# Kernel tuning notes

Measured on AMD Instinct MI355X. Metric: run time of the kernel, lower is better.

Reference implementation:

```python
import jax, jax.numpy as jnp
import numpy as np
import math

B, N, E, H, D = 8, 1024, 1024, 16, 64  # batch, node_cnt, embedding_dim, head_num, qkv_dim
SQRT_E, SQRT_D, CLIP = 32.0, 8.0, 10.0
MAX_PERIOD = 10000.0


def setup_inputs() -> dict:
    key = jax.random.key(0)
    ks = jax.random.split(key, 16)
    s = 0.03  # weight scale keeps tanh/softmax in a sane range
    return {
        "t": jax.random.uniform(ks[0], (B,), jnp.float32),
        "encoded_jobs": jax.random.normal(ks[1], (B, N, E), jnp.float32) * 0.5,
        "xt": jax.random.uniform(ks[2], (B, N, N), jnp.float32),
        "Wq": jax.random.normal(ks[3], (H * D, E), jnp.float32) * s,
        "Wk": jax.random.normal(ks[4], (H * D, E), jnp.float32) * s,
        "Wv": jax.random.normal(ks[5], (H * D, E), jnp.float32) * s,
        "Wc": jax.random.normal(ks[6], (E, H * D), jnp.float32) * s,
        "bc": jnp.zeros((E,), jnp.float32),
        "conv_w": jax.random.normal(ks[7], (2, 2), jnp.float32) * 0.5,  # 1x1 Conv2d(2,2)
        "conv_b": jnp.zeros((2,), jnp.float32),
        "tW1": jax.random.normal(ks[8], (E // 2, E), jnp.float32) * s,
        "tb1": jnp.zeros((E // 2,), jnp.float32),
        "tW2": jax.random.normal(ks[9], (E, E // 2), jnp.float32) * s,
        "tb2": jnp.zeros((E,), jnp.float32),
    }


def _timestep_embedding(t):
    half = E // 2
    freqs = jnp.exp(-math.log(MAX_PERIOD) * jnp.arange(half, dtype=jnp.float32) / half)
    args = t[:, None] * freqs[None, :]               # [B, E/2]
    return jnp.concatenate([jnp.cos(args), jnp.sin(args)], axis=-1)  # [B, E]


def reference(t, encoded_jobs, xt, Wq, Wk, Wv, Wc, bc, conv_w, conv_b, tW1, tb1, tW2, tb2):
    # time embedding MLP
    t_emb = jax.nn.relu(_timestep_embedding(t) @ tW1.T + tb1) @ tW2.T + tb2  # [B, E]

    def heads(W):
        return (encoded_jobs @ W.T).reshape(B, N, H, D).transpose(0, 2, 1, 3)  # [B,H,N,D]

    q, k, v = heads(Wq), heads(Wk), heads(Wv)
    attn = jax.nn.softmax(jnp.einsum('bhnd,bhmd->bhnm', q, k) / SQRT_D, axis=-1)
    out = jnp.einsum('bhnm,bhmd->bhnd', attn, v)
    out_concat = out.transpose(0, 2, 1, 3).reshape(B, N, H * D)
    mh = out_concat @ Wc.T + bc + t_emb[:, None, :]          # [B,N,E]

    # single-head score against encoded_jobs^T, scaled + tanh-clipped
    score = jnp.einsum('bne,bme->bnm', mh, encoded_jobs) / SQRT_E
    score_clipped = CLIP * jnp.tanh(score)

    stacked = jnp.stack([score_clipped, xt], axis=1)         # [B,2,N,N]
    conv_out = jnp.einsum('oi,binm->bonm', conv_w, stacked) + conv_b[None, :, None, None]
    return jax.nn.softmax(conv_out.transpose(0, 2, 3, 1), axis=3)  # [B,N,N,2]
```

## Files before the change

### kernel.cpp

```cpp
#include <hip/hip_runtime.h>
#include <hip/hip_bf16.h>
#include <math.h>

#define B_ 8
#define N_ 1024
#define E_ 1024
#define H_ 16
#define D_ 64

typedef __attribute__((ext_vector_type(8))) short short8;
typedef __attribute__((ext_vector_type(4))) float f32x4;

static __device__ __forceinline__ unsigned short f2bf(float f) {
    __hip_bfloat16 h = __float2bfloat16(f);
    return __builtin_bit_cast(unsigned short, h);
}
static __device__ __forceinline__ void gld_lds16(const void* g, void* l) {
    __builtin_amdgcn_global_load_lds(
        (const __attribute__((address_space(1))) unsigned int*)g,
        (__attribute__((address_space(3))) unsigned int*)l, 16, 0, 0);
}

__global__ __launch_bounds__(256) void cvt_multi(
    const float* __restrict__ s0, const float* __restrict__ s1,
    const float* __restrict__ s2, const float* __restrict__ s3,
    const float* __restrict__ s4,
    unsigned short* __restrict__ d0, unsigned short* __restrict__ d1,
    unsigned short* __restrict__ d2, unsigned short* __restrict__ d3,
    unsigned short* __restrict__ d4, int nbig, int nsmall)
{
    const int z = blockIdx.y;
    const float* s; unsigned short* d; int n;
    switch (z) {
        case 0: s = s0; d = d0; n = nbig; break;
        case 1: s = s1; d = d1; n = nsmall; break;
        case 2: s = s2; d = d2; n = nsmall; break;
        case 3: s = s3; d = d3; n = nsmall; break;
        default: s = s4; d = d4; n = nsmall; break;
    }
    int i = (blockIdx.x * 256 + threadIdx.x) * 4;
    if (i >= n) return;
    float4 v = *(const float4*)(s + i);
    *(ushort4*)(d + i) = make_ushort4(f2bf(v.x), f2bf(v.y), f2bf(v.z), f2bf(v.w));
}

__global__ __launch_bounds__(256) void temb1_kernel(
    const float* __restrict__ t, const float* __restrict__ tW1,
    const float* __restrict__ tb1, float* __restrict__ h1T)
{
    const int wv = threadIdx.x >> 6, lane = threadIdx.x & 63;
    const int j = blockIdx.x * 4 + wv;
    float tv[8];
#pragma unroll
    for (int b = 0; b < 8; ++b) tv[b] = t[b];
    const float* w = tW1 + j * 1024;
    float acc[8];
#pragma unroll
    for (int b = 0; b < 8; ++b) acc[b] = 0.f;
    const float kLog = 9.210340371976184f;
    for (int e = lane; e < 1024; e += 64) {
        float we = w[e];
        int ef = e & 511;
        float freq = __expf(-kLog * (float)ef * (1.0f / 512.0f));
        if (e < 512) {
#pragma unroll
            for (int b = 0; b < 8; ++b) acc[b] = fmaf(we, __cosf(tv[b] * freq), acc[b]);
        } else {
#pragma unroll
            for (int b = 0; b < 8; ++b) acc[b] = fmaf(we, __sinf(tv[b] * freq), acc[b]);
        }
    }
#pragma unroll
    for (int off = 32; off > 0; off >>= 1)
#pragma unroll
        for (int b = 0; b < 8; ++b) acc[b] += __shfl_xor(acc[b], off, 64);
    if (lane == 0) {
        float bias = tb1[j];
#pragma unroll
        for (int b = 0; b < 8; ++b) h1T[j * 8 + b] = fmaxf(acc[b] + bias, 0.f);
    }
}

__global__ __launch_bounds__(256) void temb2_kernel(
    const float* __restrict__ h1T, const float* __restrict__ tW2,
    const float* __restrict__ tb2, float* __restrict__ temb)
{
    const int wv = threadIdx.x >> 6, lane = threadIdx.x & 63;
    const int e2 = blockIdx.x * 4 + wv;
    const float* w = tW2 + e2 * 512;
    float acc[8];
#pragma unroll
    for (int b = 0; b < 8; ++b) acc[b] = 0.f;
    for (int j = lane; j < 512; j += 64) {
        float wv_ = w[j];
        const float* hp = h1T + j * 8;
#pragma unroll
        for (int b = 0; b < 8; ++b) acc[b] = fmaf(hp[b], wv_, acc[b]);
    }
#pragma unroll
    for (int off = 32; off > 0; off >>= 1)
#pragma unroll
        for (int b = 0; b < 8; ++b) acc[b] += __shfl_xor(acc[b], off, 64);
    if (lane == 0) {
        float bias = tb2[e2];
#pragma unroll
        for (int b = 0; b < 8; ++b) temb[b * 1024 + e2] = acc[b] + bias;
    }
}

static __device__ __forceinline__ void gemm_loop(
    const unsigned short* __restrict__ A, const unsigned short* __restrict__ Bm,
    int m0, int n0, int K,
    unsigned short* As0, unsigned short* As1,
    unsigned short* Bs0, unsigned short* Bs1,
    f32x4 acc[4][4])
{
    const int tid = threadIdx.x;
    const int wave = tid >> 6, lane = tid & 63;
    const int wm = wave >> 1, wn = wave & 1;
    const int sr = lane >> 2, sc = (lane & 3) * 8;
    const unsigned short* Ag0 = A + (size_t)(m0 + wave * 16 + sr) * K + sc;
    const unsigned short* Ag1 = A + (size_t)(m0 + 64 + wave * 16 + sr) * K + sc;
    const unsigned short* Bg0 = Bm + (size_t)(n0 + wave * 16 + sr) * K + sc;
    const unsigned short* Bg1 = Bm + (size_t)(n0 + 64 + wave * 16 + sr) * K + sc;

    const f32x4 zero = {0.f, 0.f, 0.f, 0.f};
#pragma unroll
    for (int i = 0; i < 4; ++i)
#pragma unroll
        for (int j = 0; j < 4; ++j) acc[i][j] = zero;

    gld_lds16(Ag0, As0 + wave * 512);
    gld_lds16(Ag1, As0 + (wave + 4) * 512);
    gld_lds16(Bg0, Bs0 + wave * 512);
    gld_lds16(Bg1, Bs0 + (wave + 4) * 512);
    __syncthreads();

    const int fr = lane & 15, fq = (lane >> 4) * 8;
    int cur = 0;
    for (int k0 = 0; k0 < K; k0 += 32) {
        const unsigned short* sA = cur ? As1 : As0;
        const unsigned short* sB = cur ? Bs1 : Bs0;
        unsigned short* dA = cur ? As0 : As1;
        unsigned short* dB = cur ? Bs0 : Bs1;
        if (k0 + 32 < K) {
            gld_lds16(Ag0 + k0 + 32, dA + wave * 512);
            gld_lds16(Ag1 + k0 + 32, dA + (wave + 4) * 512);
            gld_lds16(Bg0 + k0 + 32, dB + wave * 512);
            gld_lds16(Bg1 + k0 + 32, dB + (wave + 4) * 512);
        }
        short8 af[4], bf[4];
#pragma unroll
        for (int i = 0; i < 4; ++i) {
            af[i] = *(const short8*)&sA[(wm * 64 + i * 16 + fr) * 32 + fq];
            bf[i] = *(const short8*)&sB[(wn * 64 + i * 16 + fr) * 32 + fq];
        }
#pragma unroll
        for (int i = 0; i < 4; ++i)
#pragma unroll
            for (int j = 0; j < 4; ++j)
                acc[i][j] = __builtin_amdgcn_mfma_f32_16x16x32_bf16(
                    af[i], bf[j], acc[i][j], 0, 0, 0);
        __syncthreads();
        cur ^= 1;
    }
}

__global__ __launch_bounds__(256) void qkv_gemm(
    const unsigned short* __restrict__ A,
    const unsigned short* __restrict__ W0, const unsigned short* __restrict__ W1,
    const unsigned short* __restrict__ W2,
    unsigned short* __restrict__ C0, unsigned short* __restrict__ C1,
    unsigned short* __restrict__ C2)
{
    __shared__ unsigned short As0[128 * 32], As1[128 * 32];
    __shared__ unsigned short Bs0[128 * 32], Bs1[128 * 32];
    const int orig = blockIdx.x;
    const int sw = (orig & 7) * 192 + (orig >> 3);
    const int z = sw / 512, r = sw & 511;
    const int m0 = (r >> 3) * 128, n0 = (r & 7) * 128;
    const unsigned short* W = z == 0 ? W0 : (z == 1 ? W1 : W2);
    unsigned short* C = z == 0 ? C0 : (z == 1 ? C1 : C2);

    f32x4 acc[4][4];
    gemm_loop(A, W, m0, n0, 1024, As0, As1, Bs0, Bs1, acc);

    const int lane = threadIdx.x & 63, wave = threadIdx.x >> 6;
    const int wm = wave >> 1, wn = wave & 1;
    const int fr = lane & 15, fq4 = (lane >> 4) * 4;
#pragma unroll
    for (int i = 0; i < 4; ++i) {
        int row = m0 + wm * 64 + i * 16 + fq4;
#pragma unroll
        for (int j = 0; j < 4; ++j) {
            int col = n0 + wn * 64 + j * 16 + fr;
#pragma unroll
            for (int rr = 0; rr < 4; ++rr)
                C[(size_t)(row + rr) * 1024 + col] = f2bf(acc[i][j][rr]);
        }
    }
}

__global__ __launch_bounds__(256) void outproj_gemm(
    const unsigned short* __restrict__ A, const unsigned short* __restrict__ Bm,
    unsigned short* __restrict__ C,
    const float* __restrict__ bias, const float* __restrict__ temb)
{
    __shared__ unsigned short As0[128 * 32], As1[128 * 32];
    __shared__ unsigned short Bs0[128 * 32], Bs1[128 * 32];
    const int orig = blockIdx.x;
    const int sw = (orig & 7) * 64 + (orig >> 3);
    const int m0 = (sw >> 3) * 128, n0 = (sw & 7) * 128;

    f32x4 acc[4][4];
    gemm_loop(A, Bm, m0, n0, 1024, As0, As1, Bs0, Bs1, acc);

    const int lane = threadIdx.x & 63, wave = threadIdx.x >> 6;
    const int wm = wave >> 1, wn = wave & 1;
    const int fr = lane & 15, fq4 = (lane >> 4) * 4;
    const int bb = m0 >> 10;
#pragma unroll
    for (int i = 0; i < 4; ++i) {
        int row = m0 + wm * 64 + i * 16 + fq4;
#pragma unroll
        for (int j = 0; j < 4; ++j) {
            int col = n0 + wn * 64 + j * 16 + fr;
            float epi = bias[col] + temb[bb * 1024 + col];
#pragma unroll
            for (int rr = 0; rr < 4; ++rr)
                C[(size_t)(row + rr) * 1024 + col] = f2bf(acc[i][j][rr] + epi);
        }
    }
}

__global__ __launch_bounds__(256) void attn_mfma(
    const unsigned short* __restrict__ Q, const unsigned short* __restrict__ K,
    const unsigned short* __restrict__ V, unsigned short* __restrict__ O)
{
    __shared__ __align__(16) unsigned short Ks[64 * 72];
    __shared__ __align__(16) unsigned short Vts[80 * 72];
    __shared__ __align__(16) unsigned short Pl[4][32 * 72];
    const int tid = threadIdx.x;
    const int wq = tid >> 6, lane = tid & 63;
    const int lo = lane & 15, hi = lane >> 4;
    const int id = blockIdx.x;
    const int sw = (id & 7) * 128 + (id >> 3);
    const int q0 = (sw & 7) * 128;
    const int h = (sw >> 3) & 15, b = sw >> 7;
    const size_t base = ((size_t)b * N_) * 1024 + h * 64;

    for (int i = tid; i < 16 * 64; i += 256) {
        int rr = i >> 6, cc = i & 63;
        Vts[(64 + rr) * 72 + cc] = (rr == 0) ? (unsigned short)0x3F80 : (unsigned short)0;
    }

    short8 aq[2][2];
#pragma unroll
    for (int qt = 0; qt < 2; ++qt)
#pragma unroll
        for (int ks = 0; ks < 2; ++ks)
            aq[qt][ks] = *(const short8*)(Q + base +
                (size_t)(q0 + wq * 32 + qt * 16 + lo) * 1024 + hi * 8 + ks * 32);

    f32x4 o_[2][5];
    const f32x4 zero = {0.f, 0.f, 0.f, 0.f};
    float m_[2] = {-1e30f, -1e30f};
#pragma unroll
    for (int qt = 0; qt < 2; ++qt)
#pragma unroll
        for (int db = 0; db < 5; ++db) o_[qt][db] = zero;

    const int kr = tid >> 2, ku = (tid & 3) * 16;
    const unsigned short* Kg = K + base + (size_t)kr * 1024 + ku;
    const int vkv = (tid & 31) * 2, vd = (tid >> 5) * 8;
    const unsigned short* Vg = V + base + (size_t)vkv * 1024 + vd;

    short8 kl0 = *(const short8*)(Kg);
    short8 kl1 = *(const short8*)(Kg + 8);
    short8 vla = *(const short8*)(Vg);
    short8 vlb = *(const short8*)(Vg + 1024);

    const float cexp = 0.1803368801111204f;

    for (int kt = 0; kt < N_; kt += 64) {
        __syncthreads();
        *(short8*)&Ks[kr * 72 + ku] = kl0;
        *(short8*)&Ks[kr * 72 + ku + 8] = kl1;
#pragma unroll
        for (int i = 0; i < 8; ++i) {
            unsigned int pv = (unsigned int)(unsigned short)vla[i] |
                              ((unsigned int)(unsigned short)vlb[i] << 16);
            *(unsigned int*)&Vts[(vd + i) * 72 + vkv] = pv;
        }
        __syncthreads();
        if (kt + 64 < N_) {
            kl0 = *(const short8*)(Kg + (size_t)(kt + 64) * 1024);
            kl1 = *(const short8*)(Kg + (size_t)(kt + 64) * 1024 + 8);
            vla = *(const short8*)(Vg + (size_t)(kt + 64) * 1024);
            vlb = *(const short8*)(Vg + (size_t)(kt + 64) * 1024 + 1024);
        }

        short8 kb[4][2];
#pragma unroll
        for (int jk = 0; jk < 4; ++jk)
#pragma unroll
            for (int ks = 0; ks < 2; ++ks)
                kb[jk][ks] = *(const short8*)&Ks[(16 * jk + lo) * 72 + hi * 8 + ks * 32];

#pragma unroll
        for (int qt = 0; qt < 2; ++qt) {
            f32x4 s[4];
            __builtin_amdgcn_s_setprio(1);
#pragma unroll
            for (int jk = 0; jk < 4; ++jk) {
                s[jk] = __builtin_amdgcn_mfma_f32_16x16x32_bf16(
                    kb[jk][0], aq[qt][0], zero, 0, 0, 0);
                s[jk] = __builtin_amdgcn_mfma_f32_16x16x32_bf16(
                    kb[jk][1], aq[qt][1], s[jk], 0, 0, 0);
            }
            __builtin_amdgcn_s_setprio(0);
            float mx0 = fmaxf(fmaxf(s[0][0], s[0][1]), fmaxf(s[0][2], s[0][3]));
            float mx1 = fmaxf(fmaxf(s[1][0], s[1][1]), fmaxf(s[1][2], s[1][3]));
            float mx2 = fmaxf(fmaxf(s[2][0], s[2][1]), fmaxf(s[2][2], s[2][3]));
            float mx3 = fmaxf(fmaxf(s[3][0], s[3][1]), fmaxf(s[3][2], s[3][3]));
            float mx = fmaxf(fmaxf(mx0, mx1), fmaxf(mx2, mx3));
            mx = fmaxf(mx, __shfl_xor(mx, 16, 64));
            mx = fmaxf(mx, __shfl_xor(mx, 32, 64));
            if (!__all(mx <= m_[qt] + 64.f)) {
                float mn = fmaxf(m_[qt], mx);
                float scale = exp2f((m_[qt] - mn) * cexp);
                m_[qt] = mn;
#pragma unroll
                for (int db = 0; db < 5; ++db)
#pragma unroll
                    for (int rr = 0; rr < 4; ++rr) o_[qt][db][rr] *= scale;
            }
            float nm = -m_[qt] * cexp;
#pragma unroll
            for (int jk = 0; jk < 4; ++jk)
#pragma unroll
                for (int rr = 0; rr < 4; ++rr)
                    s[jk][rr] = exp2f(fmaf(s[jk][rr], cexp, nm));
#pragma unroll
            for (int jk = 0; jk < 4; ++jk) {
                unsigned int pw0 = (unsigned int)f2bf(s[jk][0]) |
                                   ((unsigned int)f2bf(s[jk][1]) << 16);
                unsigned int pw1 = (unsigned int)f2bf(s[jk][2]) |
                                   ((unsigned int)f2bf(s[jk][3]) << 16);
                *(uint2*)&Pl[wq][(qt * 16 + lo) * 72 + 16 * jk + 4 * hi] =
                    make_uint2(pw0, pw1);
            }
        }

        short8 vb[5][2], pa[2][2];
#pragma unroll
        for (int db = 0; db < 5; ++db)
#pragma unroll
            for (int k2 = 0; k2 < 2; ++k2)
                vb[db][k2] = *(const short8*)&Vts[(16 * db + lo) * 72 +
                                                  hi * 8 + k2 * 32];
#pragma unroll
        for (int qt = 0; qt < 2; ++qt)
#pragma unroll
            for (int k2 = 0; k2 < 2; ++k2)
                pa[qt][k2] = *(const short8*)&Pl[wq][(qt * 16 + lo) * 72 +
                                                     hi * 8 + k2 * 32];
        __builtin_amdgcn_s_setprio(1);
#pragma unroll
        for (int qt = 0; qt < 2; ++qt)
#pragma unroll
            for (int db = 0; db < 5; ++db) {
                o_[qt][db] = __builtin_amdgcn_mfma_f32_16x16x32_bf16(
                    vb[db][0], pa[qt][0], o_[qt][db], 0, 0, 0);
                o_[qt][db] = __builtin_amdgcn_mfma_f32_16x16x32_bf16(
                    vb[db][1], pa[qt][1], o_[qt][db], 0, 0, 0);
            }
        __builtin_amdgcn_s_setprio(0);
    }

#pragma unroll
    for (int qt = 0; qt < 2; ++qt) {
        float lsum = __shfl(o_[qt][4][0], lo, 64);
        float inv = 1.f / lsum;
        const size_t rb = base + (size_t)(q0 + wq * 32 + qt * 16 + lo) * 1024;
#pragma unroll
        for (int db = 0; db < 4; ++db) {
            *(ushort4*)(O + rb + 16 * db + 4 * hi) = make_ushort4(
                f2bf(o_[qt][db][0] * inv), f2bf(o_[qt][db][1] * inv),
                f2bf(o_[qt][db][2] * inv), f2bf(o_[qt][db][3] * inv));
        }
    }
}

__global__ __launch_bounds__(256) void score_bf16(
    const unsigned short* __restrict__ MH, const unsigned short* __restrict__ EJ,
    const float* __restrict__ xt, const float* __restrict__ convw,
    const float* __restrict__ convb, float* __restrict__ out)
{
    __shared__ unsigned short As0[128 * 32], As1[128 * 32];
    __shared__ unsigned short Bs0[128 * 32], Bs1[128 * 32];
    const int orig = blockIdx.x;
    const int sw = (orig & 7) * 64 + (orig >> 3);
    const int bz = sw >> 6;
    const int m0 = ((sw >> 3) & 7) * 128, n0 = (sw & 7) * 128;
    const unsigned short* A = MH + (size_t)bz * N_ * E_;
    const unsigned short* Bm = EJ + (size_t)bz * N_ * E_;

    f32x4 acc[4][4];
    gemm_loop(A, Bm, m0, n0, 1024, As0, As1, Bs0, Bs1, acc);

    const int lane = threadIdx.x & 63, wave = threadIdx.x >> 6;
    const int wm = wave >> 1, wn = wave & 1;
    const int fr = lane & 15, fq4 = (lane >> 4) * 4;
    const float w00 = convw[0], w01 = convw[1], w10 = convw[2], w11 = convw[3];
    const float cb0 = convb[0], cb1 = convb[1];
#pragma unroll
    for (int i = 0; i < 4; ++i) {
#pragma unroll
        for (int rr = 0; rr < 4; ++rr) {
            int row = m0 + wm * 64 + i * 16 + fq4 + rr;
            const float* xrow = xt + ((size_t)bz * N_ + row) * N_;
            float2* orow = (float2*)(out + (((size_t)bz * N_ + row) * N_) * 2);
#pragma unroll
            for (int j = 0; j < 4; ++j) {
                int col = n0 + wn * 64 + j * 16 + fr;
                float sc_ = 10.f * tanhf(acc[i][j][rr] * 0.03125f);
                float x = xrow[col];
                float c0 = fmaf(w00, sc_, fmaf(w01, x, cb0));
                float c1 = fmaf(w10, sc_, fmaf(w11, x, cb1));
                float mx = fmaxf(c0, c1);
                float e0 = __expf(c0 - mx), e1 = __expf(c1 - mx);
                float inv = 1.f / (e0 + e1);
                orow[col] = make_float2(e0 * inv, e1 * inv);
            }
        }
    }
}

extern "C" void kernel_launch(void* const* d_in, const int* in_sizes, int n_in,
                              void* d_out, int out_size, void* d_ws, size_t ws_size,
                              hipStream_t stream)
{
    (void)in_sizes; (void)n_in; (void)out_size; (void)ws_size;
    const float* t     = (const float*)d_in[0];
    const float* ej    = (const float*)d_in[1];
    const float* xt    = (const float*)d_in[2];
    const float* Wq    = (const float*)d_in[3];
    const float* Wk    = (const float*)d_in[4];
    const float* Wv    = (const float*)d_in[5];
    const float* Wc    = (const float*)d_in[6];
    const float* bc    = (const float*)d_in[7];
    const float* convw = (const float*)d_in[8];
    const float* convb = (const float*)d_in[9];
    const float* tW1   = (const float*)d_in[10];
    const float* tb1   = (const float*)d_in[11];
    const float* tW2   = (const float*)d_in[12];
    const float* tb2   = (const float*)d_in[13];
    float* out = (float*)d_out;

    const size_t SZ = (size_t)B_ * N_ * 1024;
    float* ws = (float*)d_ws;
    float* temb = ws;
    float* h1T  = ws + 8192;
    unsigned short* ej_bf = (unsigned short*)(ws + 8192 + 4096);
    unsigned short* MH_bf = ej_bf + SZ;
    unsigned short* Wq_bf = MH_bf + SZ;
    unsigned short* Wk_bf = Wq_bf + (size_t)E_ * 1024;
    unsigned short* Wv_bf = Wk_bf + (size_t)E_ * 1024;
    unsigned short* Wc_bf = Wv_bf + (size_t)E_ * 1024;

    unsigned short* Qb = (unsigned short*)d_out;
    unsigned short* Kb = Qb + SZ;
    unsigned short* Vb = Kb + SZ;
    unsigned short* Ob = Vb + SZ;

    cvt_multi<<<dim3(8192, 5), dim3(256), 0, stream>>>(
        ej, Wq, Wk, Wv, Wc, ej_bf, Wq_bf, Wk_bf, Wv_bf, Wc_bf,
        (int)SZ, E_ * 1024);
    temb1_kernel<<<dim3(128), dim3(256), 0, stream>>>(t, tW1, tb1, h1T);
    temb2_kernel<<<dim3(256), dim3(256), 0, stream>>>(h1T, tW2, tb2, temb);

    dim3 gblk(256);
    qkv_gemm<<<dim3(1536), gblk, 0, stream>>>(
        ej_bf, Wq_bf, Wk_bf, Wv_bf, Qb, Kb, Vb);

    attn_mfma<<<dim3(1024), gblk, 0, stream>>>(Qb, Kb, Vb, Ob);

    outproj_gemm<<<dim3(512), gblk, 0, stream>>>(Ob, Wc_bf, MH_bf, bc, temb);

    score_bf16<<<dim3(512), gblk, 0, stream>>>(
        MH_bf, ej_bf, xt, convw, convb, out);
}
```

Measured before the change: 245.8 us.

## Keep softmax probabilities in registers by permuting V layout in LDS

The attention kernel no longer round-trips the bf16 probability tile through a per-wave LDS buffer. Instead, the V tile is stored with a permuted key column order, so the MFMA output fragments of S can be packed directly into B-operand registers for the PV MFMA. It also uses v_cvt_pk_bf16_f32 for packing and v_permlane32_swap for the cross-half max reduction. This removes LDS writes and reads plus a dependency stall per tile, at the cost of relying on a subtle index permutation being correct.

```diff
diff --git a/kernel.cpp b/kernel.cpp
--- a/kernel.cpp
+++ b/kernel.cpp
@@ -14,6 +14,11 @@
 static __device__ __forceinline__ unsigned short f2bf(float f) {
     __hip_bfloat16 h = __float2bfloat16(f);
     return __builtin_bit_cast(unsigned short, h);
+}
+static __device__ __forceinline__ unsigned int cvtpk_bf16(float a, float b) {
+    unsigned int r;
+    asm("v_cvt_pk_bf16_f32 %0, %1, %2" : "=v"(r) : "v"(a), "v"(b));
+    return r;
 }
 static __device__ __forceinline__ void gld_lds16(const void* g, void* l) {
     __builtin_amdgcn_global_load_lds(
@@ -239,7 +244,6 @@
 {
     __shared__ __align__(16) unsigned short Ks[64 * 72];
     __shared__ __align__(16) unsigned short Vts[80 * 72];
-    __shared__ __align__(16) unsigned short Pl[4][32 * 72];
     const int tid = threadIdx.x;
     const int wq = tid >> 6, lane = tid & 63;
     const int lo = lane & 15, hi = lane >> 4;
@@ -273,6 +277,7 @@
     const int kr = tid >> 2, ku = (tid & 3) * 16;
     const unsigned short* Kg = K + base + (size_t)kr * 1024 + ku;
     const int vkv = (tid & 31) * 2, vd = (tid >> 5) * 8;
+    const int scol = (vkv & 0x23) | ((vkv & 0x0C) << 1) | ((vkv & 0x10) >> 2);
     const unsigned short* Vg = V + base + (size_t)vkv * 1024 + vd;
 
     short8 kl0 = *(const short8*)(Kg);
@@ -290,7 +295,7 @@
         for (int i = 0; i < 8; ++i) {
             unsigned int pv = (unsigned int)(unsigned short)vla[i] |
                               ((unsigned int)(unsigned short)vlb[i] << 16);
-            *(unsigned int*)&Vts[(vd + i) * 72 + vkv] = pv;
+            *(unsigned int*)&Vts[(vd + i) * 72 + scol] = pv;
         }
         __syncthreads();
         if (kt + 64 < N_) {
@@ -300,12 +305,18 @@
             vlb = *(const short8*)(Vg + (size_t)(kt + 64) * 1024 + 1024);
         }
 
-        short8 kb[4][2];
+        short8 kb[4][2], vb[5][2];
 #pragma unroll
         for (int jk = 0; jk < 4; ++jk)
 #pragma unroll
             for (int ks = 0; ks < 2; ++ks)
                 kb[jk][ks] = *(const short8*)&Ks[(16 * jk + lo) * 72 + hi * 8 + ks * 32];
+#pragma unroll
+        for (int db = 0; db < 5; ++db)
+#pragma unroll
+            for (int k2 = 0; k2 < 2; ++k2)
+                vb[db][k2] = *(const short8*)&Vts[(16 * db + lo) * 72 +
+                                                  hi * 8 + k2 * 32];
 
 #pragma unroll
         for (int qt = 0; qt < 2; ++qt) {
@@ -325,7 +336,11 @@
             float mx3 = fmaxf(fmaxf(s[3][0], s[3][1]), fmaxf(s[3][2], s[3][3]));
             float mx = fmaxf(fmaxf(mx0, mx1), fmaxf(mx2, mx3));
             mx = fmaxf(mx, __shfl_xor(mx, 16, 64));
-            mx = fmaxf(mx, __shfl_xor(mx, 32, 64));
+            {
+                float u = mx, v = mx;
+                asm("v_permlane32_swap_b32 %0, %1" : "+v"(u), "+v"(v));
+                mx = fmaxf(u, v);
+            }
             if (!__all(mx <= m_[qt] + 64.f)) {
                 float mn = fmaxf(m_[qt], mx);
                 float scale = exp2f((m_[qt] - mn) * cexp);
@@ -341,41 +356,27 @@
 #pragma unroll
                 for (int rr = 0; rr < 4; ++rr)
                     s[jk][rr] = exp2f(fmaf(s[jk][rr], cexp, nm));
+            unsigned int pw[8];
 #pragma unroll
             for (int jk = 0; jk < 4; ++jk) {
-                unsigned int pw0 = (unsigned int)f2bf(s[jk][0]) |
-                                   ((unsigned int)f2bf(s[jk][1]) << 16);
-                unsigned int pw1 = (unsigned int)f2bf(s[jk][2]) |
-                                   ((unsigned int)f2bf(s[jk][3]) << 16);
-                *(uint2*)&Pl[wq][(qt * 16 + lo) * 72 + 16 * jk + 4 * hi] =
-                    make_uint2(pw0, pw1);
-            }
-        }
-
-        short8 vb[5][2], pa[2][2];
-#pragma unroll
-        for (int db = 0; db < 5; ++db)
-#pragma unroll
-            for (int k2 = 0; k2 < 2; ++k2)
-                vb[db][k2] = *(const short8*)&Vts[(16 * db + lo) * 72 +
-                                                  hi * 8 + k2 * 32];
-#pragma unroll
-        for (int qt = 0; qt < 2; ++qt)
-#pragma unroll
-            for (int k2 = 0; k2 < 2; ++k2)
-                pa[qt][k2] = *(const short8*)&Pl[wq][(qt * 16 + lo) * 72 +
-                                                     hi * 8 + k2 * 32];
-        __builtin_amdgcn_s_setprio(1);
-#pragma unroll
-        for (int qt = 0; qt < 2; ++qt)
+                pw[2 * jk] = cvtpk_bf16(s[jk][0], s[jk][1]);
+                pw[2 * jk + 1] = cvtpk_bf16(s[jk][2], s[jk][3]);
+            }
+            uint4 pa0 = make_uint4(pw[0], pw[1], pw[2], pw[3]);
+            uint4 pa1 = make_uint4(pw[4], pw[5], pw[6], pw[7]);
+            short8 pA = __builtin_bit_cast(short8, pa0);
+            short8 pB = __builtin_bit_cast(short8, pa1);
+
+            __builtin_amdgcn_s_setprio(1);
 #pragma unroll
             for (int db = 0; db < 5; ++db) {
                 o_[qt][db] = __builtin_amdgcn_mfma_f32_16x16x32_bf16(
-                    vb[db][0], pa[qt][0], o_[qt][db], 0, 0, 0);
+                    vb[db][0], pA, o_[qt][db], 0, 0, 0);
                 o_[qt][db] = __builtin_amdgcn_mfma_f32_16x16x32_bf16(
-                    vb[db][1], pa[qt][1], o_[qt][db], 0, 0, 0);
-            }
-        __builtin_amdgcn_s_setprio(0);
+                    vb[db][1], pB, o_[qt][db], 0, 0, 0);
+            }
+            __builtin_amdgcn_s_setprio(0);
+        }
     }
 
 #pragma unroll
```

Measured after the change: 244.6 us. Within noise of the previous version (-0.5%).
